# Kernel tuning notes

Hardware: AMD Instinct MI355X
Metric: run time of the kernel (lower is better)

Reference implementation:

```python
import jax, jax.numpy as jnp
import numpy as np

EPS = 1e-05


def reference(inputs, c1, h1, c2, h2, w, b, norm_w, norm_b):
    B = inputs.shape[0]
    U = inputs.shape[1]
    # [B, 3U] @ [3U, 5U] + [1, 5U]
    x = jnp.concatenate([inputs, h1, h2], axis=1)
    res = x @ w + b
    # split into 5 contiguous gates -> [B, 5, U], layer-norm each gate over last axis
    g = res.reshape(B, 5, U)
    m = jnp.mean(g, axis=-1, keepdims=True)
    v = jnp.var(g, axis=-1, keepdims=True)  # biased variance, matches tf.nn.moments
    ln = (g - m) / jnp.sqrt(v + EPS) * norm_w[None, :, :] + norm_b[None, :, :]
    i, j, f, f2, o = ln[:, 0], ln[:, 1], ln[:, 2], ln[:, 3], ln[:, 4]
    new_c = c1 * jax.nn.sigmoid(f) + c2 * jax.nn.sigmoid(f2) + jax.nn.sigmoid(i) * jnp.tanh(j)
    new_h = new_c * jax.nn.sigmoid(o)
    return new_c, new_h


def setup_inputs() -> dict:
    B, U = 16384, 512
    key = jax.random.key(0)
    ks = jax.random.split(key, 6)
    return {
        "inputs": jax.random.normal(ks[0], (B, U), dtype=jnp.float32),
        "c1": jax.random.normal(ks[1], (B, U), dtype=jnp.float32),
        "h1": jax.random.normal(ks[2], (B, U), dtype=jnp.float32),
        "c2": jax.random.normal(ks[3], (B, U), dtype=jnp.float32),
        "h2": jax.random.normal(ks[4], (B, U), dtype=jnp.float32),
        "w": jax.random.normal(ks[5], (3 * U, 5 * U), dtype=jnp.float32) * (1.0 / np.sqrt(3 * U)),
        "b": jnp.zeros((1, 5 * U), dtype=jnp.float32),
        "norm_w": jnp.ones((5, U), dtype=jnp.float32),
        "norm_b": jnp.zeros((5, U), dtype=jnp.float32),
    }
```

## Files before the change

kernel.cpp:

```cpp
#include <hip/hip_runtime.h>
#include <hip/hip_bf16.h>
#include <cstdint>

#define B_DIM 16384
#define U_DIM 512
#define K_DIM 1536
#define N_DIM 2560

typedef unsigned short u16;
typedef __attribute__((ext_vector_type(2))) unsigned short u16x2;
typedef __attribute__((ext_vector_type(4))) unsigned short u16x4;
typedef __attribute__((ext_vector_type(8))) short bf16x8;
typedef __attribute__((ext_vector_type(4))) float f32x4;

__device__ __forceinline__ u16 f2bf(float f) {
    uint32_t u = __builtin_bit_cast(uint32_t, f);
    u += 0x7FFFu + ((u >> 16) & 1u);
    return (u16)(u >> 16);
}
__device__ __forceinline__ float bf2f(u16 h) {
    uint32_t u = ((uint32_t)h) << 16;
    return __builtin_bit_cast(float, u);
}

__global__ void __launch_bounds__(256) cvt_x_kernel(
    const float* __restrict__ inp, const float* __restrict__ h1,
    const float* __restrict__ h2, u16* __restrict__ xb)
{
    int idx = blockIdx.x * 256 + threadIdx.x;
    const int total4 = B_DIM * K_DIM / 4;
    if (idx >= total4) return;
    int e = idx * 4;
    int b = e / K_DIM;
    int k = e - b * K_DIM;
    const float* src;
    if (k < 512)       src = inp + b * 512 + k;
    else if (k < 1024) src = h1  + b * 512 + (k - 512);
    else               src = h2  + b * 512 + (k - 1024);
    float4 v = *(const float4*)src;
    u16x4 o;
    o.x = f2bf(v.x); o.y = f2bf(v.y); o.z = f2bf(v.z); o.w = f2bf(v.w);
    *(u16x4*)(xb + e) = o;
}

__global__ void __launch_bounds__(256) cvt_wT_kernel(
    const float* __restrict__ w, u16* __restrict__ wT)
{
    __shared__ float tile[32][33];
    const int n0 = blockIdx.x * 32;
    const int k0 = blockIdx.y * 32;
    const int tx = threadIdx.x & 31;
    const int ty = threadIdx.x >> 5;
#pragma unroll
    for (int i = 0; i < 4; ++i) {
        int kk = ty + i * 8;
        tile[kk][tx] = w[(k0 + kk) * N_DIM + n0 + tx];
    }
    __syncthreads();
#pragma unroll
    for (int i = 0; i < 4; ++i) {
        int nn = ty + i * 8;
        wT[(int64_t)(n0 + nn) * K_DIM + k0 + tx] = f2bf(tile[tx][nn]);
    }
}

#define BM 128
#define BN 128
#define BK 64

__device__ __forceinline__ void gload_lds16(const void* g, void* l) {
    __builtin_amdgcn_global_load_lds(
        (const __attribute__((address_space(1))) void*)g,
        (__attribute__((address_space(3))) void*)l, 16, 0, 0);
}

__global__ void __launch_bounds__(256) gemm_kernel(
    const u16* __restrict__ A, const u16* __restrict__ Bt,
    u16* __restrict__ C)
{
    __shared__ u16 As[BM * BK];
    __shared__ u16 Bs[BN * BK];

    const int tid  = threadIdx.x;
    const int lane = tid & 63;
    const int wave = tid >> 6;

    const int nwg = 2560;
    int bid = blockIdx.x;
    int swz = (bid & 7) * (nwg / 8) + (bid >> 3);
    const int by = swz / (N_DIM / BN);
    const int bx = swz % (N_DIM / BN);
    const int bm = by * BM;
    const int bn = bx * BN;

    const int wm = (wave >> 1) * 64;
    const int wn = (wave & 1) * 64;

    f32x4 acc[4][4];
#pragma unroll
    for (int i = 0; i < 4; ++i)
#pragma unroll
        for (int j = 0; j < 4; ++j) acc[i][j] = (f32x4)(0.0f);

    const int chunk0 = wave * 64 + lane;

    for (int kt = 0; kt < K_DIM; kt += BK) {
#pragma unroll
        for (int i = 0; i < 4; ++i) {
            int ch  = i * 256 + chunk0;
            int row = ch >> 3;
            int c8  = ch & 7;
            const u16* ga = A  + (int64_t)(bm + row) * K_DIM + kt + c8 * 8;
            const u16* gb = Bt + (int64_t)(bn + row) * K_DIM + kt + c8 * 8;
            char* la = (char*)As + (i * 256 + wave * 64) * 16;
            char* lb = (char*)Bs + (i * 256 + wave * 64) * 16;
            gload_lds16(ga, la);
            gload_lds16(gb, lb);
        }
        __syncthreads();

#pragma unroll
        for (int ks = 0; ks < 2; ++ks) {
            bf16x8 af[4], bfr[4];
#pragma unroll
            for (int m = 0; m < 4; ++m)
                af[m] = *(const bf16x8*)&As[(wm + m * 16 + (lane & 15)) * BK +
                                            ks * 32 + (lane >> 4) * 8];
#pragma unroll
            for (int n = 0; n < 4; ++n)
                bfr[n] = *(const bf16x8*)&Bs[(wn + n * 16 + (lane & 15)) * BK +
                                             ks * 32 + (lane >> 4) * 8];
#pragma unroll
            for (int m = 0; m < 4; ++m)
#pragma unroll
                for (int n = 0; n < 4; ++n)
                    acc[m][n] = __builtin_amdgcn_mfma_f32_16x16x32_bf16(
                        af[m], bfr[n], acc[m][n], 0, 0, 0);
        }
        __syncthreads();
    }

    const int col0 = lane & 15;
    const int row0 = (lane >> 4) * 4;
#pragma unroll
    for (int m = 0; m < 4; ++m)
#pragma unroll
        for (int n = 0; n < 4; ++n)
#pragma unroll
            for (int r = 0; r < 4; ++r) {
                int grow = bm + wm + m * 16 + row0 + r;
                int gcol = bn + wn + n * 16 + col0;
                C[(int64_t)grow * N_DIM + gcol] = f2bf(acc[m][n][r]);
            }
}

__global__ void __launch_bounds__(256) ln_pointwise_kernel(
    const u16*  __restrict__ res,  const float* __restrict__ bias,
    const float* __restrict__ c1,  const float* __restrict__ c2,
    const float* __restrict__ nw,  const float* __restrict__ nb,
    float* __restrict__ out)
{
    const int b    = blockIdx.x;
    const int t    = threadIdx.x;
    const int lane = t & 63;
    const int wave = t >> 6;

    __shared__ float2 part[5][4];

    const u16* row = res + (int64_t)b * N_DIM;
    float v[5][2];

#pragma unroll
    for (int g = 0; g < 5; ++g) {
        u16x2  raw = *(const u16x2*)(row + g * 512 + t * 2);
        float2 bb  = *(const float2*)(bias + g * 512 + t * 2);
        v[g][0] = bf2f(raw.x) + bb.x;
        v[g][1] = bf2f(raw.y) + bb.y;
        float s = v[g][0] + v[g][1];
        float q = v[g][0] * v[g][0] + v[g][1] * v[g][1];
#pragma unroll
        for (int off = 32; off >= 1; off >>= 1) {
            s += __shfl_xor(s, off);
            q += __shfl_xor(q, off);
        }
        if (lane == 0) part[g][wave] = make_float2(s, q);
    }
    __syncthreads();

    float mean[5], rstd[5];
#pragma unroll
    for (int g = 0; g < 5; ++g) {
        float s = part[g][0].x + part[g][1].x + part[g][2].x + part[g][3].x;
        float q = part[g][0].y + part[g][1].y + part[g][2].y + part[g][3].y;
        float m   = s * (1.0f / 512.0f);
        float var = q * (1.0f / 512.0f) - m * m;
        mean[g] = m;
        rstd[g] = rsqrtf(var + 1e-5f);
    }

    float lnv[5][2];
#pragma unroll
    for (int g = 0; g < 5; ++g) {
        float2 w2 = *(const float2*)(nw + g * 512 + t * 2);
        float2 b2 = *(const float2*)(nb + g * 512 + t * 2);
        lnv[g][0] = (v[g][0] - mean[g]) * rstd[g] * w2.x + b2.x;
        lnv[g][1] = (v[g][1] - mean[g]) * rstd[g] * w2.y + b2.y;
    }

    float2 c1v = *(const float2*)(c1 + (int64_t)b * 512 + t * 2);
    float2 c2v = *(const float2*)(c2 + (int64_t)b * 512 + t * 2);

#pragma unroll
    for (int e = 0; e < 2; ++e) {
        float ig  = 1.0f / (1.0f + expf(-lnv[0][e]));
        float jg  = tanhf(lnv[1][e]);
        float fg  = 1.0f / (1.0f + expf(-lnv[2][e]));
        float f2g = 1.0f / (1.0f + expf(-lnv[3][e]));
        float og  = 1.0f / (1.0f + expf(-lnv[4][e]));
        float c1s = e ? c1v.y : c1v.x;
        float c2s = e ? c2v.y : c2v.x;
        float cc = c1s * fg + c2s * f2g + ig * jg;
        float hh = cc * og;
        int64_t o = (int64_t)b * 512 + t * 2 + e;
        out[o] = cc;
        out[(int64_t)B_DIM * U_DIM + o] = hh;
    }
}

extern "C" void kernel_launch(void* const* d_in, const int* in_sizes, int n_in,
                              void* d_out, int out_size, void* d_ws, size_t ws_size,
                              hipStream_t stream)
{
    const float* inputs = (const float*)d_in[0];
    const float* c1     = (const float*)d_in[1];
    const float* h1     = (const float*)d_in[2];
    const float* c2     = (const float*)d_in[3];
    const float* h2     = (const float*)d_in[4];
    const float* w      = (const float*)d_in[5];
    const float* bias   = (const float*)d_in[6];
    const float* nw     = (const float*)d_in[7];
    const float* nb     = (const float*)d_in[8];
    float* out = (float*)d_out;

    const size_t XB_BYTES = (size_t)B_DIM * K_DIM * 2;
    const size_t WT_BYTES = (size_t)N_DIM * K_DIM * 2;
    u16* xb  = (u16*)d_ws;
    u16* wT  = (u16*)((char*)d_ws + XB_BYTES);
    u16* res = (u16*)((char*)d_ws + XB_BYTES + WT_BYTES);

    cvt_x_kernel<<<(B_DIM * K_DIM / 4 + 255) / 256, 256, 0, stream>>>(inputs, h1, h2, xb);
    cvt_wT_kernel<<<dim3(N_DIM / 32, K_DIM / 32), 256, 0, stream>>>(w, wT);
    gemm_kernel<<<(B_DIM / BM) * (N_DIM / BN), 256, 0, stream>>>(xb, wT, res);
    ln_pointwise_kernel<<<B_DIM, 256, 0, stream>>>(res, bias, c1, c2, nw, nb, out);
}
```

Baseline: 475.1 us.

## Rewrite GEMM as double-buffered 256x256 tile pipeline and vectorize LN kernel

The GEMM moves from 128x128 single-buffered tiles to 256x256 tiles with 512 threads. It double-buffers LDS with a swizzled layout and interleaves global-to-LDS prefetch of the next K-tile with MFMA work, using explicit waitcnt, barriers and setprio. The layernorm/pointwise kernel now handles one row per wave with 8-wide vector loads and stores, which removes the shared-memory cross-wave reduction. These changes target LDS bank conflicts, exposed memory latency and small per-block work, at the cost of heavy hand-scheduled synchronisation and high register pressure from 128 accumulator registers per lane.

```diff
diff --git a/kernel.cpp b/kernel.cpp
--- a/kernel.cpp
+++ b/kernel.cpp
@@ -6,10 +6,11 @@
 #define U_DIM 512
 #define K_DIM 1536
 #define N_DIM 2560
+#define NT    24
 
 typedef unsigned short u16;
-typedef __attribute__((ext_vector_type(2))) unsigned short u16x2;
 typedef __attribute__((ext_vector_type(4))) unsigned short u16x4;
+typedef __attribute__((ext_vector_type(8))) unsigned short u16x8;
 typedef __attribute__((ext_vector_type(8))) short bf16x8;
 typedef __attribute__((ext_vector_type(4))) float f32x4;
 
@@ -64,92 +65,134 @@
     }
 }
 
-#define BM 128
-#define BN 128
-#define BK 64
-
 __device__ __forceinline__ void gload_lds16(const void* g, void* l) {
     __builtin_amdgcn_global_load_lds(
         (const __attribute__((address_space(1))) void*)g,
         (__attribute__((address_space(3))) void*)l, 16, 0, 0);
 }
 
-__global__ void __launch_bounds__(256) gemm_kernel(
+#define BAR    __builtin_amdgcn_s_barrier()
+#define FENCE  asm volatile("" ::: "memory")
+#define VMCNT4 asm volatile("s_waitcnt vmcnt(4)" ::: "memory")
+#define LGKM0  do { asm volatile("s_waitcnt lgkmcnt(0)" ::: "memory"); \
+                    __builtin_amdgcn_sched_barrier(0); } while (0)
+
+__global__ void __launch_bounds__(512, 2) gemm_kernel(
     const u16* __restrict__ A, const u16* __restrict__ Bt,
     u16* __restrict__ C)
 {
-    __shared__ u16 As[BM * BK];
-    __shared__ u16 Bs[BN * BK];
+    __shared__ u16 sm[65536];
 
     const int tid  = threadIdx.x;
     const int lane = tid & 63;
     const int wave = tid >> 6;
 
-    const int nwg = 2560;
     int bid = blockIdx.x;
-    int swz = (bid & 7) * (nwg / 8) + (bid >> 3);
-    const int by = swz / (N_DIM / BN);
-    const int bx = swz % (N_DIM / BN);
-    const int bm = by * BM;
-    const int bn = bx * BN;
-
-    const int wm = (wave >> 1) * 64;
-    const int wn = (wave & 1) * 64;
-
-    f32x4 acc[4][4];
-#pragma unroll
-    for (int i = 0; i < 4; ++i)
+    int swz = (bid & 7) * 80 + (bid >> 3);
+    const int bm = (swz / 10) * 256;
+    const int bn = (swz % 10) * 256;
+
+    const int wm = (wave >> 2) * 128;
+    const int wn = (wave & 3) * 64;
+
+    const int l15 = lane & 15, cq = lane >> 4;
+    const int s   = (((l15 & 1) << 2) | cq) ^ ((l15 >> 1) & 7);
+    const int rdA = ((wm >> 1) + (l15 >> 1)) * 64 + s * 8;
+    const int rdB = ((wn >> 1) + (l15 >> 1)) * 64 + s * 8;
+
+    const int line0 = tid >> 3;
+    const int sl0   = (tid & 7) ^ (line0 & 7);
+    const int srow  = line0 * 2 + (sl0 >> 2);
+    const int sc8   = (sl0 & 3) * 8;
+    const u16* gA = A  + (int64_t)(bm + srow) * K_DIM + sc8;
+    const u16* gB = Bt + (int64_t)(bn + srow) * K_DIM + sc8;
+    char* ld0 = (char*)sm + tid * 16;
+
+#define STAGE(ab, ks, kt, buf) do {                                        \
+        const u16* g_ = ((ab) ? gB : gA) + (kt) + (ks) * 32;               \
+        char* d_ = ld0 + (buf) * 65536 + (ab) * 32768 + (ks) * 16384;      \
+        gload_lds16(g_, d_);                                               \
+        gload_lds16(g_ + 128 * K_DIM, d_ + 8192);                          \
+    } while (0)
+
+    f32x4 acc[8][4];
+#pragma unroll
+    for (int i = 0; i < 8; ++i)
 #pragma unroll
         for (int j = 0; j < 4; ++j) acc[i][j] = (f32x4)(0.0f);
 
-    const int chunk0 = wave * 64 + lane;
-
-    for (int kt = 0; kt < K_DIM; kt += BK) {
-#pragma unroll
-        for (int i = 0; i < 4; ++i) {
-            int ch  = i * 256 + chunk0;
-            int row = ch >> 3;
-            int c8  = ch & 7;
-            const u16* ga = A  + (int64_t)(bm + row) * K_DIM + kt + c8 * 8;
-            const u16* gb = Bt + (int64_t)(bn + row) * K_DIM + kt + c8 * 8;
-            char* la = (char*)As + (i * 256 + wave * 64) * 16;
-            char* lb = (char*)Bs + (i * 256 + wave * 64) * 16;
-            gload_lds16(ga, la);
-            gload_lds16(gb, lb);
-        }
-        __syncthreads();
-
-#pragma unroll
-        for (int ks = 0; ks < 2; ++ks) {
-            bf16x8 af[4], bfr[4];
-#pragma unroll
-            for (int m = 0; m < 4; ++m)
-                af[m] = *(const bf16x8*)&As[(wm + m * 16 + (lane & 15)) * BK +
-                                            ks * 32 + (lane >> 4) * 8];
-#pragma unroll
-            for (int n = 0; n < 4; ++n)
-                bfr[n] = *(const bf16x8*)&Bs[(wn + n * 16 + (lane & 15)) * BK +
-                                             ks * 32 + (lane >> 4) * 8];
-#pragma unroll
-            for (int m = 0; m < 4; ++m)
-#pragma unroll
-                for (int n = 0; n < 4; ++n)
-                    acc[m][n] = __builtin_amdgcn_mfma_f32_16x16x32_bf16(
-                        af[m], bfr[n], acc[m][n], 0, 0, 0);
-        }
-        __syncthreads();
-    }
-
-    const int col0 = lane & 15;
-    const int row0 = (lane >> 4) * 4;
-#pragma unroll
-    for (int m = 0; m < 4; ++m)
+    STAGE(0, 0, 0, 0);
+    STAGE(1, 0, 0, 0);
+    STAGE(0, 1, 0, 0);
+    STAGE(1, 1, 0, 0);
+    VMCNT4;
+    BAR; FENCE;
+
+    bf16x8 af[4], bfr[4];
+
+#define LOAD_A4(BASE) _Pragma("unroll")                                    \
+    for (int mi = 0; mi < 4; ++mi) af[mi] = *(const bf16x8*)((BASE) + mi * 512)
+#define LOAD_B4(BASE) _Pragma("unroll")                                    \
+    for (int n = 0; n < 4; ++n) bfr[n] = *(const bf16x8*)((BASE) + n * 512)
+#define MFMA16(MB) _Pragma("unroll")                                       \
+    for (int mi = 0; mi < 4; ++mi) { _Pragma("unroll")                     \
+        for (int n = 0; n < 4; ++n)                                        \
+            acc[(MB) + mi][n] = __builtin_amdgcn_mfma_f32_16x16x32_bf16(   \
+                af[mi], bfr[n], acc[(MB) + mi][n], 0, 0, 0); }
+
+    for (int t = 0; t < NT; ++t) {
+        const int cur = t & 1, nxt = cur ^ 1;
+        const int ktn = ((t + 1) == NT) ? 0 : (t + 1) * 64;
+        const u16* aB = sm + cur * 32768 + rdA;
+        const u16* bB = sm + cur * 32768 + 16384 + rdB;
+
+        LOAD_A4(aB);
+        LOAD_B4(bB);
+        STAGE(0, 0, ktn, nxt);
+        BAR; LGKM0;
+        __builtin_amdgcn_s_setprio(1);
+        MFMA16(0);
+        __builtin_amdgcn_s_setprio(0);
+        BAR; FENCE;
+
+        LOAD_A4(aB + 4 * 512);
+        STAGE(1, 0, ktn, nxt);
+        BAR; LGKM0;
+        __builtin_amdgcn_s_setprio(1);
+        MFMA16(4);
+        __builtin_amdgcn_s_setprio(0);
+        VMCNT4;
+        BAR; FENCE;
+
+        LOAD_A4(aB + 8192);
+        LOAD_B4(bB + 8192);
+        STAGE(0, 1, ktn, nxt);
+        BAR; LGKM0;
+        __builtin_amdgcn_s_setprio(1);
+        MFMA16(0);
+        __builtin_amdgcn_s_setprio(0);
+        BAR; FENCE;
+
+        LOAD_A4(aB + 8192 + 4 * 512);
+        STAGE(1, 1, ktn, nxt);
+        BAR; LGKM0;
+        __builtin_amdgcn_s_setprio(1);
+        MFMA16(4);
+        __builtin_amdgcn_s_setprio(0);
+        VMCNT4;
+        BAR; FENCE;
+    }
+
+    const int ecol = lane & 15;
+    const int erow = (lane >> 4) * 4;
+#pragma unroll
+    for (int m = 0; m < 8; ++m)
 #pragma unroll
         for (int n = 0; n < 4; ++n)
 #pragma unroll
             for (int r = 0; r < 4; ++r) {
-                int grow = bm + wm + m * 16 + row0 + r;
-                int gcol = bn + wn + n * 16 + col0;
+                int grow = bm + wm + m * 16 + erow + r;
+                int gcol = bn + wn + n * 16 + ecol;
                 C[(int64_t)grow * N_DIM + gcol] = f2bf(acc[m][n][r]);
             }
 }
@@ -160,71 +203,75 @@
     const float* __restrict__ nw,  const float* __restrict__ nb,
     float* __restrict__ out)
 {
-    const int b    = blockIdx.x;
-    const int t    = threadIdx.x;
-    const int lane = t & 63;
-    const int wave = t >> 6;
-
-    __shared__ float2 part[5][4];
-
+    const int wave = threadIdx.x >> 6;
+    const int lane = threadIdx.x & 63;
+    const int b    = blockIdx.x * 4 + wave;
     const u16* row = res + (int64_t)b * N_DIM;
-    float v[5][2];
+    const int u0 = lane * 8;
+
+    float v[5][8];
+    float rstd[5], mean[5];
 
 #pragma unroll
     for (int g = 0; g < 5; ++g) {
-        u16x2  raw = *(const u16x2*)(row + g * 512 + t * 2);
-        float2 bb  = *(const float2*)(bias + g * 512 + t * 2);
-        v[g][0] = bf2f(raw.x) + bb.x;
-        v[g][1] = bf2f(raw.y) + bb.y;
-        float s = v[g][0] + v[g][1];
-        float q = v[g][0] * v[g][0] + v[g][1] * v[g][1];
-#pragma unroll
-        for (int off = 32; off >= 1; off >>= 1) {
+        u16x8 raw = *(const u16x8*)(row + g * 512 + u0);
+        const float4* bp = (const float4*)(bias + g * 512 + u0);
+        float4 b0 = bp[0], b1 = bp[1];
+        v[g][0] = bf2f(raw[0]) + b0.x;  v[g][1] = bf2f(raw[1]) + b0.y;
+        v[g][2] = bf2f(raw[2]) + b0.z;  v[g][3] = bf2f(raw[3]) + b0.w;
+        v[g][4] = bf2f(raw[4]) + b1.x;  v[g][5] = bf2f(raw[5]) + b1.y;
+        v[g][6] = bf2f(raw[6]) + b1.z;  v[g][7] = bf2f(raw[7]) + b1.w;
+        float s = 0.f, q = 0.f;
+#pragma unroll
+        for (int j = 0; j < 8; ++j) { s += v[g][j]; q += v[g][j] * v[g][j]; }
+#pragma unroll
+        for (int off = 1; off < 64; off <<= 1) {
             s += __shfl_xor(s, off);
             q += __shfl_xor(q, off);
         }
-        if (lane == 0) part[g][wave] = make_float2(s, q);
-    }
-    __syncthreads();
-
-    float mean[5], rstd[5];
-#pragma unroll
-    for (int g = 0; g < 5; ++g) {
-        float s = part[g][0].x + part[g][1].x + part[g][2].x + part[g][3].x;
-        float q = part[g][0].y + part[g][1].y + part[g][2].y + part[g][3].y;
         float m   = s * (1.0f / 512.0f);
         float var = q * (1.0f / 512.0f) - m * m;
         mean[g] = m;
         rstd[g] = rsqrtf(var + 1e-5f);
     }
 
-    float lnv[5][2];
 #pragma unroll
     for (int g = 0; g < 5; ++g) {
-        float2 w2 = *(const float2*)(nw + g * 512 + t * 2);
-        float2 b2 = *(const float2*)(nb + g * 512 + t * 2);
-        lnv[g][0] = (v[g][0] - mean[g]) * rstd[g] * w2.x + b2.x;
-        lnv[g][1] = (v[g][1] - mean[g]) * rstd[g] * w2.y + b2.y;
-    }
-
-    float2 c1v = *(const float2*)(c1 + (int64_t)b * 512 + t * 2);
-    float2 c2v = *(const float2*)(c2 + (int64_t)b * 512 + t * 2);
-
-#pragma unroll
-    for (int e = 0; e < 2; ++e) {
-        float ig  = 1.0f / (1.0f + expf(-lnv[0][e]));
-        float jg  = tanhf(lnv[1][e]);
-        float fg  = 1.0f / (1.0f + expf(-lnv[2][e]));
-        float f2g = 1.0f / (1.0f + expf(-lnv[3][e]));
-        float og  = 1.0f / (1.0f + expf(-lnv[4][e]));
-        float c1s = e ? c1v.y : c1v.x;
-        float c2s = e ? c2v.y : c2v.x;
-        float cc = c1s * fg + c2s * f2g + ig * jg;
-        float hh = cc * og;
-        int64_t o = (int64_t)b * 512 + t * 2 + e;
-        out[o] = cc;
-        out[(int64_t)B_DIM * U_DIM + o] = hh;
-    }
+        const float4* wp = (const float4*)(nw + g * 512 + u0);
+        const float4* bp = (const float4*)(nb + g * 512 + u0);
+        float4 w0 = wp[0], w1 = wp[1], n0 = bp[0], n1 = bp[1];
+        float ws[8] = {w0.x, w0.y, w0.z, w0.w, w1.x, w1.y, w1.z, w1.w};
+        float ns[8] = {n0.x, n0.y, n0.z, n0.w, n1.x, n1.y, n1.z, n1.w};
+#pragma unroll
+        for (int j = 0; j < 8; ++j)
+            v[g][j] = (v[g][j] - mean[g]) * rstd[g] * ws[j] + ns[j];
+    }
+
+    const float4* c1p = (const float4*)(c1 + (int64_t)b * 512 + u0);
+    const float4* c2p = (const float4*)(c2 + (int64_t)b * 512 + u0);
+    float4 c1a = c1p[0], c1b = c1p[1], c2a = c2p[0], c2b = c2p[1];
+    float c1s[8] = {c1a.x, c1a.y, c1a.z, c1a.w, c1b.x, c1b.y, c1b.z, c1b.w};
+    float c2s[8] = {c2a.x, c2a.y, c2a.z, c2a.w, c2b.x, c2b.y, c2b.z, c2b.w};
+
+    float oc[8], oh[8];
+#pragma unroll
+    for (int j = 0; j < 8; ++j) {
+        float ig  = 1.0f / (1.0f + expf(-v[0][j]));
+        float jg  = tanhf(v[1][j]);
+        float fg  = 1.0f / (1.0f + expf(-v[2][j]));
+        float f2g = 1.0f / (1.0f + expf(-v[3][j]));
+        float og  = 1.0f / (1.0f + expf(-v[4][j]));
+        float cc  = c1s[j] * fg + c2s[j] * f2g + ig * jg;
+        oc[j] = cc;
+        oh[j] = cc * og;
+    }
+
+    float* oC = out + (int64_t)b * 512 + u0;
+    float* oH = out + (int64_t)B_DIM * U_DIM + (int64_t)b * 512 + u0;
+    ((float4*)oC)[0] = make_float4(oc[0], oc[1], oc[2], oc[3]);
+    ((float4*)oC)[1] = make_float4(oc[4], oc[5], oc[6], oc[7]);
+    ((float4*)oH)[0] = make_float4(oh[0], oh[1], oh[2], oh[3]);
+    ((float4*)oH)[1] = make_float4(oh[4], oh[5], oh[6], oh[7]);
 }
 
 extern "C" void kernel_launch(void* const* d_in, const int* in_sizes, int n_in,
@@ -250,6 +297,6 @@
 
     cvt_x_kernel<<<(B_DIM * K_DIM / 4 + 255) / 256, 256, 0, stream>>>(inputs, h1, h2, xb);
     cvt_wT_kernel<<<dim3(N_DIM / 32, K_DIM / 32), 256, 0, stream>>>(w, wT);
-    gemm_kernel<<<(B_DIM / BM) * (N_DIM / BN), 256, 0, stream>>>(xb, wT, res);
-    ln_pointwise_kernel<<<B_DIM, 256, 0, stream>>>(res, bias, c1, c2, nw, nb, out);
-}
+    gemm_kernel<<<(B_DIM / 256) * (N_DIM / 256), 512, 0, stream>>>(xb, wT, res);
+    ln_pointwise_kernel<<<B_DIM / 4, 256, 0, stream>>>(res, bias, c1, c2, nw, nb, out);
+}
```

New measurement: 391.6 us. 1.21x faster.
